# Performance work log

Measured on AMD Instinct MI355X. Metric: run time of the kernel, lower is better.

## Reference

```python
import jax, jax.numpy as jnp
import numpy as np


def setup_inputs() -> dict:
    key = jax.random.key(0)
    ks = jax.random.split(key, 6)
    N, Tx, Ty = 8, 1024, 128
    enc_dim, dec_dim, Ca = 512, 1024, 128
    sc = 0.02
    return {
        "h": jax.random.normal(ks[0], (N, Tx, enc_dim), jnp.float32),
        "s": jax.random.normal(ks[1], (N, Ty, dec_dim), jnp.float32),
        "Wh": jax.random.normal(ks[2], (enc_dim, Ca), jnp.float32) * sc,
        "Ws": jax.random.normal(ks[3], (dec_dim, Ca), jnp.float32) * sc,
        "b": jax.random.normal(ks[4], (Ca,), jnp.float32) * sc,
        "v": jax.random.normal(ks[5], (Ca,), jnp.float32) * sc,
    }


def reference(h, s, Wh, Ws, b, v):
    # W([h;s]) + b == h@Wh + s@Ws + b (split of the concat Linear weight)
    ph = jnp.einsum("nxc,ca->nxa", h, Wh)            # (N, Tx, Ca)
    ps = jnp.einsum("nyd,da->nya", s, Ws) + b        # (N, Ty, Ca)
    # broadcast-add -> tanh -> dot with v : (N, Ty, Tx)
    e = jnp.einsum("nyxa,a->nyx", jnp.tanh(ps[:, :, None, :] + ph[:, None, :, :]), v)
    return jax.nn.softmax(e, axis=-1)                # attention over Tx
```

## Files before the change

kernel.cpp:

```cpp
#include <hip/hip_runtime.h>
#include <stdint.h>


typedef float  f32x4  __attribute__((ext_vector_type(4)));
typedef __bf16 bf16x8 __attribute__((ext_vector_type(8)));

#define LOG2E     1.4426950408889634f
#define TWO_LOG2E 2.8853900817779268f

__global__ void __launch_bounds__(256) transpose_cast(
    const float* __restrict__ Wh, const float* __restrict__ Ws,
    __bf16* __restrict__ WhT, __bf16* __restrict__ WsT)
{
    int bid = blockIdx.x;
    const float* src; __bf16* dst; int K, c0;
    if (bid < 8) { src = Wh; dst = WhT; K = 512;  c0 = bid * 64; }
    else         { src = Ws; dst = WsT; K = 1024; c0 = (bid - 8) * 64; }
    __shared__ float tile[64][129];
    int t = threadIdx.x;
    for (int i = 0; i < 8192; i += 256) {
        int idx = i + t;
        int r = idx >> 7, col = idx & 127;
        tile[r][col] = src[(size_t)(c0 + r) * 128 + col];
    }
    __syncthreads();
    for (int i = 0; i < 8192; i += 256) {
        int idx = i + t;
        int a = idx >> 6, cc = idx & 63;
        dst[(size_t)a * K + c0 + cc] = (__bf16)tile[cc][a];
    }
}

__global__ void __launch_bounds__(256) gemm_fused(
    const __bf16* __restrict__ WhT, const __bf16* __restrict__ WsT,
    const float* __restrict__ h, const float* __restrict__ s,
    float* __restrict__ Eph, float* __restrict__ psPart)
{
    int bid = blockIdx.x;
    int tid = threadIdx.x, lane = tid & 63, w = tid >> 6;
    int mq = w * 32;
    int q = lane >> 4, c = lane & 15;

    const __bf16* A; const float* B; float* Cp; int K, kbase, colg; bool isPs;
    if (bid < 512) {
        isPs = false; A = WhT; B = h; K = 512; kbase = 0;
        colg = bid * 16;
        int n = colg >> 10, x = colg & 1023;
        Cp = Eph + (size_t)n * 131072 + x;
    } else {
        isPs = true; A = WsT; B = s; K = 1024;
        int b2 = bid - 512;
        int half = b2 & 1; kbase = half * 512;
        colg = (b2 >> 1) * 16;
        Cp = psPart + (size_t)half * 131072 + colg;
    }

    const float*  Bp = B + (size_t)(colg + c) * K + kbase + q * 8;
    const __bf16* Ap = A + (size_t)(mq + c) * K + kbase + q * 8;

    f32x4 acc0 = {}, acc1 = {};
    float4 b0s[4], b1s[4];
    bf16x8 a0s[4], a1s[4];
    #pragma unroll
    for (int p = 0; p < 4; ++p) {
        int k = p * 32;
        b0s[p] = *(const float4*)(Bp + k);
        b1s[p] = *(const float4*)(Bp + k + 4);
        a0s[p] = *(const bf16x8*)(Ap + k);
        a1s[p] = *(const bf16x8*)(Ap + (size_t)16 * K + k);
    }
    #pragma unroll
    for (int it = 0; it < 16; ++it) {
        int cur = it & 3;
        float4 b0 = b0s[cur], b1 = b1s[cur];
        bf16x8 bf;
        bf[0] = (__bf16)b0.x; bf[1] = (__bf16)b0.y;
        bf[2] = (__bf16)b0.z; bf[3] = (__bf16)b0.w;
        bf[4] = (__bf16)b1.x; bf[5] = (__bf16)b1.y;
        bf[6] = (__bf16)b1.z; bf[7] = (__bf16)b1.w;
        acc0 = __builtin_amdgcn_mfma_f32_16x16x32_bf16(a0s[cur], bf, acc0, 0, 0, 0);
        acc1 = __builtin_amdgcn_mfma_f32_16x16x32_bf16(a1s[cur], bf, acc1, 0, 0, 0);
        if (it + 4 < 16) {
            int k = (it + 4) * 32;
            b0s[cur] = *(const float4*)(Bp + k);
            b1s[cur] = *(const float4*)(Bp + k + 4);
            a0s[cur] = *(const bf16x8*)(Ap + k);
            a1s[cur] = *(const bf16x8*)(Ap + (size_t)16 * K + k);
        }
    }

    #pragma unroll
    for (int i = 0; i < 2; ++i) {
        f32x4 av = i ? acc1 : acc0;
        #pragma unroll
        for (int r = 0; r < 4; ++r) {
            int m = mq + i * 16 + q * 4 + r;
            if (isPs) Cp[(size_t)m * 1024 + c] = av[r];
            else      Cp[(size_t)m * 1024 + c] =
                          __builtin_amdgcn_exp2f(av[r] * TWO_LOG2E);
        }
    }
}

__global__ void __launch_bounds__(512) attn_softmax(
    const float* __restrict__ Eph, const float* __restrict__ psPart,
    const float* __restrict__ bias, const float* __restrict__ v,
    float* __restrict__ out)
{
    int bid = blockIdx.x;
    int n = bid >> 6, yg = bid & 63;
    int ny = n * 128 + yg * 2;
    const float2* ph2 = (const float2*)(Eph + (size_t)n * 131072);
    int t = threadIdx.x;

    __shared__ float4 pv_s[128];
    __shared__ float wred[2][8];
    __shared__ float VsumS;

    if (t < 128) {
        float2 pa = *(const float2*)(psPart + (size_t)t * 1024 + ny);
        float2 pb = *(const float2*)(psPart + 131072 + (size_t)t * 1024 + ny);
        float bb = bias[t];
        float4 pk;
        pk.x = __builtin_amdgcn_exp2f((pa.x + pb.x + bb) * TWO_LOG2E);
        pk.y = __builtin_amdgcn_exp2f((pa.y + pb.y + bb) * TWO_LOG2E);
        pk.z = v[t]; pk.w = 0.f;
        pv_s[t] = pk;
    }
    if (t >= 448) {
        int l = t - 448;
        float vv = v[l] + v[l + 64];
        for (int m = 32; m; m >>= 1) vv += __shfl_xor(vv, m);
        if (l == 0) VsumS = vv;
    }
    __syncthreads();
    float Vsum = VsumS;

    float acc00 = 0.f, acc01 = 0.f, acc10 = 0.f, acc11 = 0.f;
    #pragma unroll 2
    for (int a = 0; a < 128; a += 4) {
        float4 q0 = pv_s[a + 0], q1 = pv_s[a + 1];
        float4 q2 = pv_s[a + 2], q3 = pv_s[a + 3];
        float2 p0 = ph2[(a + 0) * 512 + t];
        float2 p1 = ph2[(a + 1) * 512 + t];
        float2 p2 = ph2[(a + 2) * 512 + t];
        float2 p3 = ph2[(a + 3) * 512 + t];
        auto comb = [&](float e0, float e1, float e2, float e3,
                        float h0, float h1, float h2, float h3, float& acc) {
            float w0 = fmaf(e0, h0, 1.f);
            float w1 = fmaf(e1, h1, 1.f);
            float w2 = fmaf(e2, h2, 1.f);
            float w3 = fmaf(e3, h3, 1.f);
            float d01 = w0 * w1, d23 = w2 * w3;
            float n01 = fmaf(q1.z, w0, q0.z * w1);
            float n23 = fmaf(q3.z, w2, q2.z * w3);
            float dd = d01 * d23;
            float nn = fmaf(n23, d01, n01 * d23);
            acc = fmaf(nn, __builtin_amdgcn_rcpf(dd), acc);
        };
        comb(q0.x, q1.x, q2.x, q3.x, p0.x, p1.x, p2.x, p3.x, acc00);
        comb(q0.x, q1.x, q2.x, q3.x, p0.y, p1.y, p2.y, p3.y, acc01);
        comb(q0.y, q1.y, q2.y, q3.y, p0.x, p1.x, p2.x, p3.x, acc10);
        comb(q0.y, q1.y, q2.y, q3.y, p0.y, p1.y, p2.y, p3.y, acc11);
    }
    float e00 = fmaf(-2.f, acc00, Vsum);
    float e01 = fmaf(-2.f, acc01, Vsum);
    float e10 = fmaf(-2.f, acc10, Vsum);
    float e11 = fmaf(-2.f, acc11, Vsum);

    int lane = t & 63, wv = t >> 6;
    float mx0 = fmaxf(e00, e01), mx1 = fmaxf(e10, e11);
    for (int m = 32; m; m >>= 1) {
        mx0 = fmaxf(mx0, __shfl_xor(mx0, m));
        mx1 = fmaxf(mx1, __shfl_xor(mx1, m));
    }
    if (lane == 0) { wred[0][wv] = mx0; wred[1][wv] = mx1; }
    __syncthreads();
    mx0 = wred[0][0]; mx1 = wred[1][0];
    #pragma unroll
    for (int i = 1; i < 8; ++i) {
        mx0 = fmaxf(mx0, wred[0][i]);
        mx1 = fmaxf(mx1, wred[1][i]);
    }
    __syncthreads();
    float s00 = __builtin_amdgcn_exp2f((e00 - mx0) * LOG2E);
    float s01 = __builtin_amdgcn_exp2f((e01 - mx0) * LOG2E);
    float s10 = __builtin_amdgcn_exp2f((e10 - mx1) * LOG2E);
    float s11 = __builtin_amdgcn_exp2f((e11 - mx1) * LOG2E);
    float sm0 = s00 + s01, sm1 = s10 + s11;
    for (int m = 32; m; m >>= 1) {
        sm0 += __shfl_xor(sm0, m);
        sm1 += __shfl_xor(sm1, m);
    }
    if (lane == 0) { wred[0][wv] = sm0; wred[1][wv] = sm1; }
    __syncthreads();
    sm0 = 0.f; sm1 = 0.f;
    #pragma unroll
    for (int i = 0; i < 8; ++i) { sm0 += wred[0][i]; sm1 += wred[1][i]; }
    float r0 = __builtin_amdgcn_rcpf(sm0);
    float r1 = __builtin_amdgcn_rcpf(sm1);
    float2 o0; o0.x = s00 * r0; o0.y = s01 * r0;
    float2 o1; o1.x = s10 * r1; o1.y = s11 * r1;
    ((float2*)(out + (size_t)(ny + 0) * 1024))[t] = o0;
    ((float2*)(out + (size_t)(ny + 1) * 1024))[t] = o1;
}

extern "C" void kernel_launch(void* const* d_in, const int* in_sizes, int n_in,
                              void* d_out, int out_size, void* d_ws, size_t ws_size,
                              hipStream_t stream) {
    const float* h  = (const float*)d_in[0];
    const float* s  = (const float*)d_in[1];
    const float* Wh = (const float*)d_in[2];
    const float* Ws = (const float*)d_in[3];
    const float* b  = (const float*)d_in[4];
    const float* v  = (const float*)d_in[5];
    float* out = (float*)d_out;

    char* ws = (char*)d_ws;
    float*  Eph    = (float*)ws;
    float*  psPart = (float*)(ws + (4u << 20));
    __bf16* WhT    = (__bf16*)(ws + (5u << 20));
    __bf16* WsT    = WhT + (size_t)128 * 512;

    transpose_cast<<<24, 256, 0, stream>>>(Wh, Ws, WhT, WsT);
    gemm_fused<<<640, 256, 0, stream>>>(WhT, WsT, h, s, Eph, psPart);
    attn_softmax<<<512, 512, 0, stream>>>(Eph, psPart, b, v, out);
}
```

Measured before the change: 118.9 us.

## Process four decoder rows per softmax block and split weight transpose finer

Each attention block now handles four y rows instead of two. Every ph load from global memory is reused across four rows, and the block count is halved. The ph and LDS loads for the next group of four are issued ahead of the current computation, a register software pipeline, and v is moved into its own LDS array. The transpose kernel uses 96 smaller blocks instead of 24 to spread the work across more CUs. The cost is more registers per thread, which may lower occupancy, and only 256 attention blocks to fill the device.

```diff
diff --git a/kernel.cpp b/kernel.cpp
--- a/kernel.cpp
+++ b/kernel.cpp
@@ -14,19 +14,21 @@
 {
     int bid = blockIdx.x;
     const float* src; __bf16* dst; int K, c0;
-    if (bid < 8) { src = Wh; dst = WhT; K = 512;  c0 = bid * 64; }
-    else         { src = Ws; dst = WsT; K = 1024; c0 = (bid - 8) * 64; }
-    __shared__ float tile[64][129];
+    if (bid < 32) { src = Wh; dst = WhT; K = 512;  c0 = bid * 16; }
+    else          { src = Ws; dst = WsT; K = 1024; c0 = (bid - 32) * 16; }
+    __shared__ float tile[16][129];
     int t = threadIdx.x;
-    for (int i = 0; i < 8192; i += 256) {
+    #pragma unroll
+    for (int i = 0; i < 2048; i += 256) {
         int idx = i + t;
         int r = idx >> 7, col = idx & 127;
         tile[r][col] = src[(size_t)(c0 + r) * 128 + col];
     }
     __syncthreads();
-    for (int i = 0; i < 8192; i += 256) {
+    #pragma unroll
+    for (int i = 0; i < 2048; i += 256) {
         int idx = i + t;
-        int a = idx >> 6, cc = idx & 63;
+        int a = idx >> 4, cc = idx & 15;
         dst[(size_t)a * K + c0 + cc] = (__bf16)tile[cc][a];
     }
 }
@@ -108,24 +110,27 @@
     float* __restrict__ out)
 {
     int bid = blockIdx.x;
-    int n = bid >> 6, yg = bid & 63;
-    int ny = n * 128 + yg * 2;
+    int n = bid & 7, yg = bid >> 3;
+    int ny = n * 128 + yg * 4;
     const float2* ph2 = (const float2*)(Eph + (size_t)n * 131072);
     int t = threadIdx.x;
 
-    __shared__ float4 pv_s[128];
-    __shared__ float wred[2][8];
+    __shared__ f32x4 eps4[128];
+    __shared__ f32x4 vv4[32];
+    __shared__ float wred[4][8];
     __shared__ float VsumS;
 
     if (t < 128) {
-        float2 pa = *(const float2*)(psPart + (size_t)t * 1024 + ny);
-        float2 pb = *(const float2*)(psPart + 131072 + (size_t)t * 1024 + ny);
+        f32x4 pa = *(const f32x4*)(psPart + (size_t)t * 1024 + ny);
+        f32x4 pb = *(const f32x4*)(psPart + 131072 + (size_t)t * 1024 + ny);
         float bb = bias[t];
-        float4 pk;
-        pk.x = __builtin_amdgcn_exp2f((pa.x + pb.x + bb) * TWO_LOG2E);
-        pk.y = __builtin_amdgcn_exp2f((pa.y + pb.y + bb) * TWO_LOG2E);
-        pk.z = v[t]; pk.w = 0.f;
-        pv_s[t] = pk;
+        f32x4 pk;
+        #pragma unroll
+        for (int j = 0; j < 4; ++j)
+            pk[j] = __builtin_amdgcn_exp2f((pa[j] + pb[j] + bb) * TWO_LOG2E);
+        eps4[t] = pk;
+    } else if (t < 160) {
+        vv4[t - 128] = *(const f32x4*)(v + (t - 128) * 4);
     }
     if (t >= 448) {
         int l = t - 448;
@@ -136,73 +141,101 @@
     __syncthreads();
     float Vsum = VsumS;
 
-    float acc00 = 0.f, acc01 = 0.f, acc10 = 0.f, acc11 = 0.f;
+    float acc[4][2] = {};
+    float2 p[4]; f32x4 q[4]; f32x4 vr;
+    #pragma unroll
+    for (int i = 0; i < 4; ++i) p[i] = ph2[i * 512 + t];
+    #pragma unroll
+    for (int i = 0; i < 4; ++i) q[i] = eps4[i];
+    vr = vv4[0];
+
+    auto comb = [&](float e0, float e1, float e2, float e3,
+                    float h0, float h1, float h2, float h3,
+                    float v0, float v1, float v2, float v3, float& a_) {
+        float w0 = fmaf(e0, h0, 1.f);
+        float w1 = fmaf(e1, h1, 1.f);
+        float w2 = fmaf(e2, h2, 1.f);
+        float w3 = fmaf(e3, h3, 1.f);
+        float d01 = w0 * w1, d23 = w2 * w3;
+        float n01 = fmaf(v1, w0, v0 * w1);
+        float n23 = fmaf(v3, w2, v2 * w3);
+        float dd = d01 * d23;
+        float nn = fmaf(n23, d01, n01 * d23);
+        a_ = fmaf(nn, __builtin_amdgcn_rcpf(dd), a_);
+    };
+
     #pragma unroll 2
     for (int a = 0; a < 128; a += 4) {
-        float4 q0 = pv_s[a + 0], q1 = pv_s[a + 1];
-        float4 q2 = pv_s[a + 2], q3 = pv_s[a + 3];
-        float2 p0 = ph2[(a + 0) * 512 + t];
-        float2 p1 = ph2[(a + 1) * 512 + t];
-        float2 p2 = ph2[(a + 2) * 512 + t];
-        float2 p3 = ph2[(a + 3) * 512 + t];
-        auto comb = [&](float e0, float e1, float e2, float e3,
-                        float h0, float h1, float h2, float h3, float& acc) {
-            float w0 = fmaf(e0, h0, 1.f);
-            float w1 = fmaf(e1, h1, 1.f);
-            float w2 = fmaf(e2, h2, 1.f);
-            float w3 = fmaf(e3, h3, 1.f);
-            float d01 = w0 * w1, d23 = w2 * w3;
-            float n01 = fmaf(q1.z, w0, q0.z * w1);
-            float n23 = fmaf(q3.z, w2, q2.z * w3);
-            float dd = d01 * d23;
-            float nn = fmaf(n23, d01, n01 * d23);
-            acc = fmaf(nn, __builtin_amdgcn_rcpf(dd), acc);
-        };
-        comb(q0.x, q1.x, q2.x, q3.x, p0.x, p1.x, p2.x, p3.x, acc00);
-        comb(q0.x, q1.x, q2.x, q3.x, p0.y, p1.y, p2.y, p3.y, acc01);
-        comb(q0.y, q1.y, q2.y, q3.y, p0.x, p1.x, p2.x, p3.x, acc10);
-        comb(q0.y, q1.y, q2.y, q3.y, p0.y, p1.y, p2.y, p3.y, acc11);
-    }
-    float e00 = fmaf(-2.f, acc00, Vsum);
-    float e01 = fmaf(-2.f, acc01, Vsum);
-    float e10 = fmaf(-2.f, acc10, Vsum);
-    float e11 = fmaf(-2.f, acc11, Vsum);
+        int an = (a + 4 < 128) ? a + 4 : a;
+        float2 np[4]; f32x4 nq[4];
+        #pragma unroll
+        for (int i = 0; i < 4; ++i) np[i] = ph2[(an + i) * 512 + t];
+        #pragma unroll
+        for (int i = 0; i < 4; ++i) nq[i] = eps4[an + i];
+        f32x4 nvr = vv4[an >> 2];
+
+        #pragma unroll
+        for (int j = 0; j < 4; ++j) {
+            comb(q[0][j], q[1][j], q[2][j], q[3][j],
+                 p[0].x, p[1].x, p[2].x, p[3].x,
+                 vr[0], vr[1], vr[2], vr[3], acc[j][0]);
+            comb(q[0][j], q[1][j], q[2][j], q[3][j],
+                 p[0].y, p[1].y, p[2].y, p[3].y,
+                 vr[0], vr[1], vr[2], vr[3], acc[j][1]);
+        }
+        #pragma unroll
+        for (int i = 0; i < 4; ++i) { p[i] = np[i]; q[i] = nq[i]; }
+        vr = nvr;
+    }
+
+    float e[4][2];
+    #pragma unroll
+    for (int j = 0; j < 4; ++j) {
+        e[j][0] = fmaf(-2.f, acc[j][0], Vsum);
+        e[j][1] = fmaf(-2.f, acc[j][1], Vsum);
+    }
 
     int lane = t & 63, wv = t >> 6;
-    float mx0 = fmaxf(e00, e01), mx1 = fmaxf(e10, e11);
-    for (int m = 32; m; m >>= 1) {
-        mx0 = fmaxf(mx0, __shfl_xor(mx0, m));
-        mx1 = fmaxf(mx1, __shfl_xor(mx1, m));
-    }
-    if (lane == 0) { wred[0][wv] = mx0; wred[1][wv] = mx1; }
-    __syncthreads();
-    mx0 = wred[0][0]; mx1 = wred[1][0];
-    #pragma unroll
-    for (int i = 1; i < 8; ++i) {
-        mx0 = fmaxf(mx0, wred[0][i]);
-        mx1 = fmaxf(mx1, wred[1][i]);
-    }
-    __syncthreads();
-    float s00 = __builtin_amdgcn_exp2f((e00 - mx0) * LOG2E);
-    float s01 = __builtin_amdgcn_exp2f((e01 - mx0) * LOG2E);
-    float s10 = __builtin_amdgcn_exp2f((e10 - mx1) * LOG2E);
-    float s11 = __builtin_amdgcn_exp2f((e11 - mx1) * LOG2E);
-    float sm0 = s00 + s01, sm1 = s10 + s11;
-    for (int m = 32; m; m >>= 1) {
-        sm0 += __shfl_xor(sm0, m);
-        sm1 += __shfl_xor(sm1, m);
-    }
-    if (lane == 0) { wred[0][wv] = sm0; wred[1][wv] = sm1; }
-    __syncthreads();
-    sm0 = 0.f; sm1 = 0.f;
-    #pragma unroll
-    for (int i = 0; i < 8; ++i) { sm0 += wred[0][i]; sm1 += wred[1][i]; }
-    float r0 = __builtin_amdgcn_rcpf(sm0);
-    float r1 = __builtin_amdgcn_rcpf(sm1);
-    float2 o0; o0.x = s00 * r0; o0.y = s01 * r0;
-    float2 o1; o1.x = s10 * r1; o1.y = s11 * r1;
-    ((float2*)(out + (size_t)(ny + 0) * 1024))[t] = o0;
-    ((float2*)(out + (size_t)(ny + 1) * 1024))[t] = o1;
+    float mx[4];
+    #pragma unroll
+    for (int j = 0; j < 4; ++j) {
+        mx[j] = fmaxf(e[j][0], e[j][1]);
+        for (int m = 32; m; m >>= 1) mx[j] = fmaxf(mx[j], __shfl_xor(mx[j], m));
+    }
+    if (lane == 0) {
+        #pragma unroll
+        for (int j = 0; j < 4; ++j) wred[j][wv] = mx[j];
+    }
+    __syncthreads();
+    #pragma unroll
+    for (int j = 0; j < 4; ++j) {
+        mx[j] = wred[j][0];
+        #pragma unroll
+        for (int i = 1; i < 8; ++i) mx[j] = fmaxf(mx[j], wred[j][i]);
+    }
+    __syncthreads();
+    float sx[4][2], sm[4];
+    #pragma unroll
+    for (int j = 0; j < 4; ++j) {
+        sx[j][0] = __builtin_amdgcn_exp2f((e[j][0] - mx[j]) * LOG2E);
+        sx[j][1] = __builtin_amdgcn_exp2f((e[j][1] - mx[j]) * LOG2E);
+        sm[j] = sx[j][0] + sx[j][1];
+        for (int m = 32; m; m >>= 1) sm[j] += __shfl_xor(sm[j], m);
+    }
+    if (lane == 0) {
+        #pragma unroll
+        for (int j = 0; j < 4; ++j) wred[j][wv] = sm[j];
+    }
+    __syncthreads();
+    #pragma unroll
+    for (int j = 0; j < 4; ++j) {
+        float smj = 0.f;
+        #pragma unroll
+        for (int i = 0; i < 8; ++i) smj += wred[j][i];
+        float r = __builtin_amdgcn_rcpf(smj);
+        float2 o; o.x = sx[j][0] * r; o.y = sx[j][1] * r;
+        ((float2*)(out + (size_t)(ny + j) * 1024))[t] = o;
+    }
 }
 
 extern "C" void kernel_launch(void* const* d_in, const int* in_sizes, int n_in,
@@ -222,7 +255,7 @@
     __bf16* WhT    = (__bf16*)(ws + (5u << 20));
     __bf16* WsT    = WhT + (size_t)128 * 512;
 
-    transpose_cast<<<24, 256, 0, stream>>>(Wh, Ws, WhT, WsT);
+    transpose_cast<<<96, 256, 0, stream>>>(Wh, Ws, WhT, WsT);
     gemm_fused<<<640, 256, 0, stream>>>(WhT, WsT, h, s, Eph, psPart);
-    attn_softmax<<<512, 512, 0, stream>>>(Eph, psPart, b, v, out);
-}
+    attn_softmax<<<256, 512, 0, stream>>>(Eph, psPart, b, v, out);
+}
```

Result: faster. 116.5 us (-2.0%).
